# Kernel optimization log

Hardware: AMD Instinct MI355X
Metric: run time of the kernel (lower is better)

The kernel has to match this reference:

```python
import jax, jax.numpy as jnp
import numpy as np

NU, NN, NS = 50000, 20000, 2000
D_IN, D_HID, D_OUT = 128, 128, 64
LRELU_SLOPE = 0.01  # torch F.leaky_relu default


def _edges(k, n_src, n_dst, e):
    k1, k2 = jax.random.split(k)
    return (jax.random.randint(k1, (e,), 0, n_src, dtype=jnp.int32),
            jax.random.randint(k2, (e,), 0, n_dst, dtype=jnp.int32))


def setup_inputs() -> dict:
    key = jax.random.key(0)
    ks = jax.random.split(key, 32)
    fs, fd = _edges(ks[0], NU, NU, 500000)
    ps, pd = _edges(ks[1], NU, NN, 300000)
    pbs, pbd = _edges(ks[2], NN, NU, 300000)
    us, ud = _edges(ks[3], NS, NN, 150000)
    ubs, ubd = _edges(ks[4], NN, NS, 150000)
    s = 0.05
    inp = {
        "x_user": jax.random.normal(ks[5], (NU, D_IN), jnp.float32),
        "x_news": jax.random.normal(ks[6], (NN, D_IN), jnp.float32),
        "x_source": jax.random.normal(ks[7], (NS, D_IN), jnp.float32),
        # stacked per-relation GraphConv params, order:
        # [follows, posts, posted_by, publishes, published_by]
        "W1": jax.random.normal(ks[8], (5, D_IN, D_HID), jnp.float32) * s,
        "b1": jnp.zeros((5, D_HID), jnp.float32),
        "W2": jax.random.normal(ks[9], (5, D_HID, D_HID), jnp.float32) * s,
        "b2": jnp.zeros((5, D_HID), jnp.float32),
        "Wu": jax.random.normal(ks[10], (D_HID, D_OUT), jnp.float32) * s,
        "bu": jnp.zeros((D_OUT,), jnp.float32),
        "Wn": jax.random.normal(ks[11], (D_HID, D_OUT), jnp.float32) * s,
        "bn": jnp.zeros((D_OUT,), jnp.float32),
        "Ws": jax.random.normal(ks[12], (D_HID, D_OUT), jnp.float32) * s,
        "bs": jnp.zeros((D_OUT,), jnp.float32),
        "follows_src": fs, "follows_dst": fd,
        "posts_src": ps, "posts_dst": pd,
        "postedby_src": pbs, "postedby_dst": pbd,
        "publishes_src": us, "publishes_dst": ud,
        "publishedby_src": ubs, "publishedby_dst": ubd,
    }
    return inp


def _gconv(x_src, src, dst, n_dst, W, b):
    """DGL GraphConv, norm='both': D_dst^-1/2 A D_src^-1/2 X W + b."""
    n_src = x_src.shape[0]
    ones = jnp.ones(src.shape[0], x_src.dtype)
    dout = jnp.clip(jax.ops.segment_sum(ones, src, num_segments=n_src), 1.0)
    din = jnp.clip(jax.ops.segment_sum(ones, dst, num_segments=n_dst), 1.0)
    h = (x_src * jax.lax.rsqrt(dout)[:, None]) @ W  # transform before gather
    agg = jax.ops.segment_sum(h[src], dst, num_segments=n_dst)
    return agg * jax.lax.rsqrt(din)[:, None] + b


def _hetero_layer(xu, xn, xs, E, W, b):
    # mean aggregation across relations sharing a dst type
    hu = 0.5 * (_gconv(xu, E["fs"], E["fd"], NU, W[0], b[0])
                + _gconv(xn, E["pbs"], E["pbd"], NU, W[2], b[2]))
    hn = 0.5 * (_gconv(xu, E["ps"], E["pd"], NN, W[1], b[1])
                + _gconv(xs, E["us"], E["ud"], NN, W[3], b[3]))
    hs = _gconv(xn, E["ubs"], E["ubd"], NS, W[4], b[4])
    return hu, hn, hs


def reference(x_user, x_news, x_source, W1, b1, W2, b2, Wu, bu, Wn, bn, Ws, bs,
              follows_src, follows_dst, posts_src, posts_dst,
              postedby_src, postedby_dst, publishes_src, publishes_dst,
              publishedby_src, publishedby_dst):
    E = {"fs": follows_src, "fd": follows_dst, "ps": posts_src, "pd": posts_dst,
         "pbs": postedby_src, "pbd": postedby_dst, "us": publishes_src,
         "ud": publishes_dst, "ubs": publishedby_src, "ubd": publishedby_dst}
    lrelu = lambda v: jax.nn.leaky_relu(v, LRELU_SLOPE)
    hu, hn, hs = _hetero_layer(x_user, x_news, x_source, E, W1, b1)
    hu, hn, hs = lrelu(hu), lrelu(hn), lrelu(hs)
    hu, hn, hs = _hetero_layer(hu, hn, hs, E, W2, b2)
    hu, hn, hs = lrelu(hu), lrelu(hn), lrelu(hs)
    ou = hu @ Wu + bu
    on = hn @ Wn + bn
    os_ = hs @ Ws + bs
    return (ou, on, os_, hu, hn, hs)
```

## Files before the change

### kernel.cpp

```cpp
#include <hip/hip_runtime.h>

#define LRELU 0.01f

static const int kNU = 50000, kNN = 20000, kNS = 2000;
static const int DOUT_OFF[5] = {0, 100000, 170000, 240000, 262000};
static const int DIN_OFF[5]  = {50000, 150000, 190000, 242000, 282000};
static const int RP_OFF[5]   = {0, 50001, 70002, 120003, 140004};
static const int CSR_OFF[5]  = {0, 500000, 800000, 1100000, 1250000};

using bf16x8 = __attribute__((ext_vector_type(8))) short;
using u16x8  = __attribute__((ext_vector_type(8))) unsigned short;
using f32x4  = __attribute__((ext_vector_type(4))) float;

__device__ __forceinline__ float bf2f(unsigned short u) {
  return __uint_as_float(((unsigned)u) << 16);
}
__device__ __forceinline__ unsigned short f2bf(float f) {
  unsigned u = __float_as_uint(f);
  u += 0x7FFFu + ((u >> 16) & 1u);
  return (unsigned short)(u >> 16);
}


struct HArgs { const int* esrc[5]; const int* edst[5]; int* pos; int* partial; };

__global__ __launch_bounds__(512) void k_hist(HArgs a) {
  __shared__ int hbin[8192];
  int bx = blockIdx.x;
  int t = threadIdx.x;
  if (bx < 336) {
    constexpr int DSTART[6] = {0, 112, 160, 272, 320, 336};
    constexpr int NDT[5] = {50000, 20000, 50000, 20000, 2000};
    constexpr int CS[5]  = {31250, 18750, 18750, 9375, 9375};
    constexpr int EE[5]  = {500000, 300000, 300000, 150000, 150000};
    constexpr int PB[5]  = {0, 800000, 1120000, 1920000, 2240000};
    constexpr int COFF[5] = {0, 500000, 800000, 1100000, 1250000};
    int r = 0;
    while (bx >= DSTART[r + 1]) ++r;
    int local = bx - DSTART[r];
    int g = local / 16, c = local % 16;
    int nd = NDT[r];
    int gbase = g * 8192;
    int gend = gbase + 8192 < nd ? gbase + 8192 : nd;
    const int* dst = a.edst[r];
    int* pos = a.pos + COFF[r];
    int elo = c * CS[r];
    int ehi = elo + CS[r] < EE[r] ? elo + CS[r] : EE[r];
    for (int j = t; j < 8192; j += 512) hbin[j] = 0;
    __syncthreads();
    int span = ehi - elo;
    int efull = elo + (span / 4096) * 4096;
    for (int b = elo + t; b < efull; b += 4096) {
      int d[8];
#pragma unroll
      for (int k = 0; k < 8; ++k) d[k] = dst[b + k * 512];
#pragma unroll
      for (int k = 0; k < 8; ++k)
        if (d[k] >= gbase && d[k] < gend)
          pos[b + k * 512] = atomicAdd(&hbin[d[k] - gbase], 1);
    }
    for (int e = efull + t; e < ehi; e += 512) {
      int d = dst[e];
      if (d >= gbase && d < gend) pos[e] = atomicAdd(&hbin[d - gbase], 1);
    }
    __syncthreads();
    int* out = a.partial + PB[r] + (size_t)c * nd + gbase;
    int nn = gend - gbase;
    for (int j = t; j < nn; j += 512) out[j] = hbin[j];
  } else {
    constexpr int OSTART[6] = {0, 112, 224, 272, 288, 336};
    constexpr int NST[5] = {50000, 50000, 20000, 2000, 20000};
    constexpr int CS[5]  = {31250, 18750, 18750, 9375, 9375};
    constexpr int EE[5]  = {500000, 300000, 300000, 150000, 150000};
    constexpr int PB[5]  = {2272000, 3072000, 3872000, 4192000, 4224000};
    int idx = bx - 336;
    int r = 0;
    while (idx >= OSTART[r + 1]) ++r;
    int local = idx - OSTART[r];
    int g = local / 16, c = local % 16;
    int ns = NST[r];
    int gbase = g * 8192;
    int gend = gbase + 8192 < ns ? gbase + 8192 : ns;
    const int* src = a.esrc[r];
    int elo = c * CS[r];
    int ehi = elo + CS[r] < EE[r] ? elo + CS[r] : EE[r];
    for (int j = t; j < 8192; j += 512) hbin[j] = 0;
    __syncthreads();
    int span = ehi - elo;
    int efull = elo + (span / 4096) * 4096;
    for (int b = elo + t; b < efull; b += 4096) {
      int s[8];
#pragma unroll
      for (int k = 0; k < 8; ++k) s[k] = src[b + k * 512];
#pragma unroll
      for (int k = 0; k < 8; ++k)
        if (s[k] >= gbase && s[k] < gend) atomicAdd(&hbin[s[k] - gbase], 1);
    }
    for (int e = efull + t; e < ehi; e += 512) {
      int s = src[e];
      if (s >= gbase && s < gend) atomicAdd(&hbin[s - gbase], 1);
    }
    __syncthreads();
    int* out = a.partial + PB[r] + (size_t)c * ns + gbase;
    int nn = gend - gbase;
    for (int j = t; j < nn; j += 512) out[j] = hbin[j];
  }
}


struct BArgs { int* partial; int* cnt; float* rs; };

__global__ __launch_bounds__(256) void k_scanB(BArgs a) {
  int bx = blockIdx.x;
  int t = threadIdx.x;
  if (bx < 555) {
    int i = bx * 256 + t;
    if (i >= 142000) return;
    constexpr int NDT[5] = {50000, 20000, 50000, 20000, 2000};
    constexpr int PB[5]  = {0, 800000, 1120000, 1920000, 2240000};
    constexpr int DOFF[5] = {50000, 150000, 190000, 242000, 282000};
    int r, d;
    if      (i < 50000)  { r = 0; d = i; }
    else if (i < 70000)  { r = 1; d = i - 50000; }
    else if (i < 120000) { r = 2; d = i - 70000; }
    else if (i < 140000) { r = 3; d = i - 120000; }
    else                 { r = 4; d = i - 140000; }
    int nd = NDT[r];
    int* p = a.partial + PB[r] + d;
    int run = 0;
#pragma unroll
    for (int c = 0; c < 16; ++c) {
      int v = p[(size_t)c * nd];
      p[(size_t)c * nd] = run;
      run += v;
    }
    a.cnt[DOFF[r] + d] = run;
    a.rs[DOFF[r] + d] = rsqrtf((float)(run > 1 ? run : 1));
  } else {
    int i = (bx - 555) * 256 + t;
    if (i >= 142000) return;
    constexpr int NST[5] = {50000, 50000, 20000, 2000, 20000};
    constexpr int PB[5]  = {2272000, 3072000, 3872000, 4192000, 4224000};
    constexpr int OOFF[5] = {0, 100000, 170000, 240000, 262000};
    int r, s;
    if      (i < 50000)  { r = 0; s = i; }
    else if (i < 100000) { r = 1; s = i - 50000; }
    else if (i < 120000) { r = 2; s = i - 100000; }
    else if (i < 122000) { r = 3; s = i - 120000; }
    else                 { r = 4; s = i - 122000; }
    int ns = NST[r];
    const int* p = a.partial + PB[r] + s;
    int sum = 0;
#pragma unroll
    for (int c = 0; c < 16; ++c) sum += p[(size_t)c * ns];
    a.rs[OOFF[r] + s] = rsqrtf((float)(sum > 1 ? sum : 1));
  }
}


struct S3Args { const int* cnt; int* rp; };

__global__ __launch_bounds__(256) void k_scan3(S3Args a) {
  constexpr int CSTART[6] = {0, 49, 69, 118, 138, 140};
  constexpr int NDT[5] = {50000, 20000, 50000, 20000, 2000};
  constexpr int DOFF[5] = {50000, 150000, 190000, 242000, 282000};
  constexpr int RPOFF[5] = {0, 50001, 70002, 120003, 140004};
  int bx = blockIdx.x, r = 0;
  while (bx >= CSTART[r + 1]) ++r;
  int chunk = bx - CSTART[r];
  int nch = CSTART[r + 1] - CSTART[r];
  int n = NDT[r];
  const int* cnt = a.cnt + DOFF[r];
  int* rp = a.rp + RPOFF[r];
  int t = threadIdx.x;
  __shared__ int sd[256];
  __shared__ int choff_sh;
  int lim = chunk * 1024;
  int pre = 0;
  for (int j = t; j < lim; j += 256) pre += cnt[j];
  sd[t] = pre;
  __syncthreads();
  for (int off = 128; off > 0; off >>= 1) {
    if (t < off) sd[t] += sd[t + off];
    __syncthreads();
  }
  if (t == 0) choff_sh = sd[0];
  __syncthreads();
  int idx0 = lim + t * 4;
  int v[4];
#pragma unroll
  for (int j = 0; j < 4; ++j) v[j] = (idx0 + j < n) ? cnt[idx0 + j] : 0;
  int tsum = v[0] + v[1] + v[2] + v[3];
  sd[t] = tsum;
  __syncthreads();
  for (int s = 1; s < 256; s <<= 1) {
    int add = (t >= s) ? sd[t - s] : 0;
    __syncthreads();
    sd[t] += add;
    __syncthreads();
  }
  int off = choff_sh + sd[t] - tsum;
#pragma unroll
  for (int j = 0; j < 4; ++j) {
    if (idx0 + j < n) rp[idx0 + j] = off;
    off += v[j];
  }
  if (chunk == nch - 1 && t == 255) rp[n] = choff_sh + sd[255];
}


struct TJob { const float* X; const float* W; unsigned short* Y; int M; };
struct PrepJob { const float* W0; const float* W128; unsigned short* hi;
                 unsigned short* lo; int NOUT; int lgK; int bstart; };
struct CXArgs { const int* esrc[5]; const int* edst[5]; const int* pos;
                const int* rp; const int* partial; int* csr;
                TJob tj[5]; PrepJob pj[6]; };

__device__ __forceinline__ void transform_body(const TJob& p, int bxl, int t) {
  int w = t >> 6, l = t & 63;
  int lo16 = l & 15, hi4 = l >> 4;
  int m0 = bxl * 64;
  int M = p.M;
  f32x4 acc[4][2] = {};
  for (int s = 0; s < 4; ++s) {
    int kbase = s * 32 + hi4 * 8;
    bf16x8 af[4];
#pragma unroll
    for (int mf = 0; mf < 4; ++mf) {
      int row = m0 + mf * 16 + lo16;
      row = row < M ? row : M - 1;
      const float* xr = &p.X[(size_t)row * 128 + kbase];
      float4 xa = *(const float4*)xr;
      float4 xb = *(const float4*)(xr + 4);
      af[mf][0] = (short)f2bf(xa.x); af[mf][1] = (short)f2bf(xa.y);
      af[mf][2] = (short)f2bf(xa.z); af[mf][3] = (short)f2bf(xa.w);
      af[mf][4] = (short)f2bf(xb.x); af[mf][5] = (short)f2bf(xb.y);
      af[mf][6] = (short)f2bf(xb.z); af[mf][7] = (short)f2bf(xb.w);
    }
#pragma unroll
    for (int nf = 0; nf < 2; ++nf) {
      int n = (w * 2 + nf) * 16 + lo16;
      bf16x8 bh, bl;
#pragma unroll
      for (int j = 0; j < 8; ++j) {
        float wv = p.W[(size_t)(kbase + j) * 128 + n];
        unsigned short h = f2bf(wv);
        bh[j] = (short)h;
        bl[j] = (short)f2bf(wv - bf2f(h));
      }
#pragma unroll
      for (int mf = 0; mf < 4; ++mf) {
        acc[mf][nf] = __builtin_amdgcn_mfma_f32_16x16x32_bf16(af[mf], bh, acc[mf][nf], 0, 0, 0);
        acc[mf][nf] = __builtin_amdgcn_mfma_f32_16x16x32_bf16(af[mf], bl, acc[mf][nf], 0, 0, 0);
      }
    }
  }
#pragma unroll
  for (int nf = 0; nf < 2; ++nf) {
    int col = (w * 2 + nf) * 16 + lo16;
#pragma unroll
    for (int mf = 0; mf < 4; ++mf) {
#pragma unroll
      for (int rr = 0; rr < 4; ++rr) {
        int row = m0 + mf * 16 + hi4 * 4 + rr;
        if (row < M) p.Y[(size_t)row * 128 + col] = f2bf(acc[mf][nf][rr]);
      }
    }
  }
}

__global__ __launch_bounds__(256) void k_buildCx(CXArgs a) {
  int bx = blockIdx.x;
  int t = threadIdx.x;
  int g = bx / 3, m = bx % 3;
  if (m == 0) {
    constexpr int ESTART[6] = {0, 489, 782, 1075, 1222, 1369};
    constexpr int NDT[5] = {50000, 20000, 50000, 20000, 2000};
    constexpr int CS[5]  = {31250, 18750, 18750, 9375, 9375};
    constexpr int EE[5]  = {500000, 300000, 300000, 150000, 150000};
    constexpr int PB[5]  = {0, 800000, 1120000, 1920000, 2240000};
    constexpr int RPOFF[5] = {0, 50001, 70002, 120003, 140004};
    constexpr int COFF[5] = {0, 500000, 800000, 1100000, 1250000};
    int idx = g;
    if (idx >= 1369) return;
    int r = 0;
    while (idx >= ESTART[r + 1]) ++r;
    int i0 = (idx - ESTART[r]) * 1024 + t;
    const int* edst = a.edst[r];
    const int* esrc = a.esrc[r];
    const int* pos = a.pos + COFF[r];
    const int* rp = a.rp + RPOFF[r];
    const int* pb = a.partial + PB[r];
    int* csr = a.csr + COFF[r];
    int E = EE[r], cs = CS[r], nd = NDT[r];
    int i[4], d[4];
    bool v[4];
#pragma unroll
    for (int k = 0; k < 4; ++k) {
      i[k] = i0 + k * 256;
      v[k] = i[k] < E;
      d[k] = v[k] ? edst[i[k]] : 0;
    }
    int slot[4];
#pragma unroll
    for (int k = 0; k < 4; ++k) {
      if (v[k]) {
        int c = i[k] / cs;
        slot[k] = rp[d[k]] + pb[(size_t)c * nd + d[k]] + pos[i[k]];
      }
    }
#pragma unroll
    for (int k = 0; k < 4; ++k)
      if (v[k]) csr[slot[k]] = esrc[i[k]];
  } else {
    int idx = g * 2 + (m - 1);
    if (idx < 2222) {
      constexpr int TSTART[6] = {0, 782, 1564, 1877, 1909, 2222};
      int r = 0;
      while (idx >= TSTART[r + 1]) ++r;
      transform_body(a.tj[r], idx - TSTART[r], t);
    } else if (idx < 2638) {
      int b = idx - 2222, ji = 0;
      while (ji < 5 && b >= a.pj[ji + 1].bstart) ++ji;
      PrepJob p = a.pj[ji];
      int eidx = (b - p.bstart) * 256 + t;
      int K = 1 << p.lgK;
      int n = eidx >> p.lgK, k = eidx & (K - 1);
      if (n >= p.NOUT) return;
      float w = (k < 128) ? p.W0[k * p.NOUT + n] : p.W128[(k - 128) * p.NOUT + n];
      unsigned short h = f2bf(w);
      float res = w - bf2f(h);
      p.hi[n * K + k] = h;
      p.lo[n * K + k] = f2bf(res);
    }
  }
}


#define GROW(vv, cc)                                                              \
  _Pragma("unroll") for (int q = 0; q < 8; ++q)                                   \
      acc[q] = fmaf(__uint_as_float(((unsigned)(unsigned short)vv[q]) << 16), cc, acc[q]);

__device__ __forceinline__ void gat_accum(const int* __restrict__ rp,
    const int* __restrict__ csr, const unsigned short* __restrict__ Y,
    const float* __restrict__ rso, int wid, int sub, float* acc) {
  int e0 = rp[wid], e1 = rp[wid + 1];
  for (int base = e0; base < e1; base += 16) {
    int m = e1 - base;
    if (m > 16) m = 16;
    int ei = base + (sub < m ? sub : 0);
    int se = csr[ei];
    float sc = (sub < m) ? rso[se] : 0.f;
    bf16x8 v[16];
#pragma unroll
    for (int j = 0; j < 16; ++j) {
      int sj = __shfl(se, j, 16);
      v[j] = *(const bf16x8*)&Y[(size_t)sj * 128 + sub * 8];
    }
#pragma unroll
    for (int j = 0; j < 16; ++j) {
      float cj = __shfl(sc, j, 16);
      GROW(v[j], cj)
    }
  }
}


struct G1Rel { const int* rp; const int* csr; const unsigned short* Y;
               const float* rso; const float* rsi; };
struct G1Args { G1Rel rel[5]; const float* b;
                unsigned short* hU; unsigned short* hN; unsigned short* hS; };

__global__ __launch_bounds__(256) void k_gather1(G1Args a) {
  int bx = blockIdx.x;
  int t = threadIdx.x;
  int sub = t & 15;
  float acc[8], tot[8];
#pragma unroll
  for (int q = 0; q < 8; ++q) acc[q] = 0.f;
  if (bx < 3125) {
    int wid = bx * 16 + (t >> 4);
    gat_accum(a.rel[0].rp, a.rel[0].csr, a.rel[0].Y, a.rel[0].rso, wid, sub, acc);
    float s0 = a.rel[0].rsi[wid];
#pragma unroll
    for (int q = 0; q < 8; ++q) { tot[q] = s0 * acc[q]; acc[q] = 0.f; }
    gat_accum(a.rel[2].rp, a.rel[2].csr, a.rel[2].Y, a.rel[2].rso, wid, sub, acc);
    float s2 = a.rel[2].rsi[wid];
    const float* b0 = a.b;
    const float* b2 = a.b + 2 * 128;
    u16x8 o;
#pragma unroll
    for (int q = 0; q < 8; ++q) {
      float v = 0.5f * (tot[q] + s2 * acc[q] + b0[sub * 8 + q] + b2[sub * 8 + q]);
      v = v >= 0.f ? v : LRELU * v;
      o[q] = f2bf(v);
    }
    *(u16x8*)&a.hU[(size_t)wid * 128 + sub * 8] = o;
  } else if (bx < 4375) {
    int wid = (bx - 3125) * 16 + (t >> 4);
    gat_accum(a.rel[1].rp, a.rel[1].csr, a.rel[1].Y, a.rel[1].rso, wid, sub, acc);
    float s1 = a.rel[1].rsi[wid];
#pragma unroll
    for (int q = 0; q < 8; ++q) { tot[q] = s1 * acc[q]; acc[q] = 0.f; }
    gat_accum(a.rel[3].rp, a.rel[3].csr, a.rel[3].Y, a.rel[3].rso, wid, sub, acc);
    float s3 = a.rel[3].rsi[wid];
    const float* b1v = a.b + 128;
    const float* b3 = a.b + 3 * 128;
    u16x8 o;
#pragma unroll
    for (int q = 0; q < 8; ++q) {
      float v = 0.5f * (tot[q] + s3 * acc[q] + b1v[sub * 8 + q] + b3[sub * 8 + q]);
      v = v >= 0.f ? v : LRELU * v;
      o[q] = f2bf(v);
    }
    *(u16x8*)&a.hN[(size_t)wid * 128 + sub * 8] = o;
  } else {
    int wid = (bx - 4375) * 16 + (t >> 4);
    gat_accum(a.rel[4].rp, a.rel[4].csr, a.rel[4].Y, a.rel[4].rso, wid, sub, acc);
    float s4 = a.rel[4].rsi[wid];
    const float* b4 = a.b + 4 * 128;
    u16x8 o;
#pragma unroll
    for (int q = 0; q < 8; ++q) {
      float v = s4 * acc[q] + b4[sub * 8 + q];
      v = v >= 0.f ? v : LRELU * v;
      o[q] = f2bf(v);
    }
    *(u16x8*)&a.hS[(size_t)wid * 128 + sub * 8] = o;
  }
}


struct GMJob {
  const int* rpA; const int* csrA; const unsigned short* YA;
  const float* rsoA; const float* rsiA;
  const int* rpB; const int* csrB; const unsigned short* YB;
  const float* rsoB; const float* rsiB;
  const unsigned short* Wh; const unsigned short* Wl;
  const float* b0; const float* b1; float scale;
  float* H; unsigned short* Hb; int M; int KP;
};
struct GMArgs { GMJob j[3]; };

__global__ __launch_bounds__(512) void k_gmm(GMArgs a) {
  __shared__ unsigned short As[64 * 256];
  int bx = blockIdx.x;
  int ji, bxl;
  if (bx < 782)       { ji = 0; bxl = bx; }
  else if (bx < 1095) { ji = 1; bxl = bx - 782; }
  else                { ji = 2; bxl = bx - 1095; }
  const GMJob& p = a.j[ji];
  int t = threadIdx.x;
  int m0 = bxl * 64;
  char* asb = (char*)As;
  int sub = t & 15;
  int rowloc = t >> 4;
  for (int half = 0; half < 2; ++half) {
    int rl = rowloc + half * 32;
    int wid = m0 + rl;
    bool ok = wid < p.M;
    {
      float acc[8];
#pragma unroll
      for (int q = 0; q < 8; ++q) acc[q] = 0.f;
      float si = 0.f;
      if (ok) { gat_accum(p.rpA, p.csrA, p.YA, p.rsoA, wid, sub, acc); si = p.rsiA[wid]; }
      u16x8 o;
#pragma unroll
      for (int q = 0; q < 8; ++q) o[q] = f2bf(acc[q] * si);
      int cb = sub * 16;
      *(u16x8*)(asb + rl * 512 + (cb ^ ((rl & 7) << 4))) = o;
    }
    if (p.rpB) {
      float acc[8];
#pragma unroll
      for (int q = 0; q < 8; ++q) acc[q] = 0.f;
      float si = 0.f;
      if (ok) { gat_accum(p.rpB, p.csrB, p.YB, p.rsoB, wid, sub, acc); si = p.rsiB[wid]; }
      u16x8 o;
#pragma unroll
      for (int q = 0; q < 8; ++q) o[q] = f2bf(acc[q] * si);
      int cb = 256 + sub * 16;
      *(u16x8*)(asb + rl * 512 + (cb ^ ((rl & 7) << 4))) = o;
    }
  }
  __syncthreads();
  int w = t >> 6, l = t & 63;
  int lo16 = l & 15, hi4 = l >> 4;
  int KP = p.KP;
  f32x4 acc[4] = {};
  for (int s = 0; s < KP / 32; ++s) {
    int kbase = s * 32 + hi4 * 8;
    int cb = kbase * 2;
    bf16x8 af[4];
#pragma unroll
    for (int mf = 0; mf < 4; ++mf) {
      int row = mf * 16 + lo16;
      af[mf] = *(const bf16x8*)(asb + row * 512 + (cb ^ ((row & 7) << 4)));
    }
    int n = w * 16 + lo16;
    bf16x8 bh = *(const bf16x8*)&p.Wh[(size_t)n * KP + kbase];
    bf16x8 bl = *(const bf16x8*)&p.Wl[(size_t)n * KP + kbase];
#pragma unroll
    for (int mf = 0; mf < 4; ++mf) {
      acc[mf] = __builtin_amdgcn_mfma_f32_16x16x32_bf16(af[mf], bh, acc[mf], 0, 0, 0);
      acc[mf] = __builtin_amdgcn_mfma_f32_16x16x32_bf16(af[mf], bl, acc[mf], 0, 0, 0);
    }
  }
  int col = w * 16 + lo16;
  float bs = p.b0[col];
  if (p.b1) bs += p.b1[col];
#pragma unroll
  for (int mf = 0; mf < 4; ++mf) {
#pragma unroll
    for (int rr = 0; rr < 4; ++rr) {
      int row = m0 + mf * 16 + hi4 * 4 + rr;
      if (row < p.M) {
        float o = p.scale * (acc[mf][rr] + bs);
        o = o >= 0.f ? o : LRELU * o;
        p.H[(size_t)row * 128 + col] = o;
        p.Hb[(size_t)row * 128 + col] = f2bf(o);
      }
    }
  }
}


struct MJob { const unsigned short* A; const unsigned short* Wh; const unsigned short* Wl;
              const float* b0; const float* b1; float scale; int lrelu;
              float* H; int ldh; unsigned short* Hb; int M; int bstart; };
struct MArgs { MJob j[3]; };

template <int KCH, int NW>
__device__ __forceinline__ void mgemm_body(const MJob& p, int bxl) {
  constexpr int KP = KCH * 128;
  int t = threadIdx.x;
  int w = t >> 6, l = t & 63;
  int lo16 = l & 15, hi4 = l >> 4;
  int m0 = bxl * 64;
  int M = p.M;
  const unsigned short* A = p.A;
  f32x4 acc[4][NW] = {};
  for (int s = 0; s < KP / 32; ++s) {
    int kbase = s * 32 + hi4 * 8;
    bf16x8 af[4];
#pragma unroll
    for (int mf = 0; mf < 4; ++mf) {
      int row = m0 + mf * 16 + lo16;
      row = row < M ? row : M - 1;
      af[mf] = *(const bf16x8*)&A[(size_t)row * KP + kbase];
    }
#pragma unroll
    for (int nf = 0; nf < NW; ++nf) {
      int n = (w * NW + nf) * 16 + lo16;
      bf16x8 bh = *(const bf16x8*)&p.Wh[(size_t)n * KP + kbase];
      bf16x8 bl = *(const bf16x8*)&p.Wl[(size_t)n * KP + kbase];
#pragma unroll
      for (int mf = 0; mf < 4; ++mf) {
        acc[mf][nf] = __builtin_amdgcn_mfma_f32_16x16x32_bf16(af[mf], bh, acc[mf][nf], 0, 0, 0);
        acc[mf][nf] = __builtin_amdgcn_mfma_f32_16x16x32_bf16(af[mf], bl, acc[mf][nf], 0, 0, 0);
      }
    }
  }
#pragma unroll
  for (int nf = 0; nf < NW; ++nf) {
    int col = (w * NW + nf) * 16 + lo16;
    float bs = p.b0 ? p.b0[col] : 0.f;
    if (p.b1) bs += p.b1[col];
#pragma unroll
    for (int mf = 0; mf < 4; ++mf) {
#pragma unroll
      for (int rr = 0; rr < 4; ++rr) {
        int row = m0 + mf * 16 + hi4 * 4 + rr;
        if (row < M) {
          float o = p.scale * (acc[mf][nf][rr] + bs);
          if (p.lrelu) o = o >= 0.f ? o : LRELU * o;
          if (p.H) p.H[(size_t)row * p.ldh + col] = o;
          if (p.Hb) p.Hb[(size_t)row * p.ldh + col] = f2bf(o);
        }
      }
    }
  }
}

__global__ __launch_bounds__(256) void k_proj3(MArgs a) {
  int bx = blockIdx.x;
  if (bx < a.j[1].bstart)      mgemm_body<1, 1>(a.j[0], bx);
  else if (bx < a.j[2].bstart) mgemm_body<1, 1>(a.j[1], bx - a.j[1].bstart);
  else                         mgemm_body<1, 1>(a.j[2], bx - a.j[2].bstart);
}


extern "C" void kernel_launch(void* const* d_in, const int* in_sizes, int n_in,
                              void* d_out, int out_size, void* d_ws, size_t ws_size,
                              hipStream_t stream) {
  const float* xu = (const float*)d_in[0];
  const float* xn = (const float*)d_in[1];
  const float* xs = (const float*)d_in[2];
  const float* W1 = (const float*)d_in[3];
  const float* b1 = (const float*)d_in[4];
  const float* W2 = (const float*)d_in[5];
  const float* b2 = (const float*)d_in[6];
  const float* Wu = (const float*)d_in[7];
  const float* bu = (const float*)d_in[8];
  const float* Wn = (const float*)d_in[9];
  const float* bn = (const float*)d_in[10];
  const float* Wsrc = (const float*)d_in[11];
  const float* bsrc = (const float*)d_in[12];
  const int* SRC[5] = {(const int*)d_in[13], (const int*)d_in[15], (const int*)d_in[17],
                       (const int*)d_in[19], (const int*)d_in[21]};
  const int* DST[5] = {(const int*)d_in[14], (const int*)d_in[16], (const int*)d_in[18],
                       (const int*)d_in[20], (const int*)d_in[22]};

  int* ws_i = (int*)d_ws;
  int* rp = ws_i;
  int* csr = ws_i + 142008;
  int* pos = ws_i + 1542008;
  int* cnt = ws_i + 2942328;
  float* rs = (float*)(ws_i + 3226328);
  unsigned short* wt = (unsigned short*)(rs + 284000);
  unsigned short* h2bU = wt + 376832;
  unsigned short* h2bN = h2bU + 6400000;
  unsigned short* h2bS = h2bN + 2560000;
  unsigned short* xbU = wt + 376832 + 18176000;
  unsigned short* xbN = xbU + 6400000;
  unsigned short* xbS = xbN + 2560000;

  unsigned short* L2U_h = wt + 163840, * L2U_l = wt + 196608;
  unsigned short* L2N_h = wt + 229376, * L2N_l = wt + 262144;
  unsigned short* L2S_h = wt + 294912, * L2S_l = wt + 311296;
  unsigned short* PU_h = wt + 327680, * PU_l = wt + 335872;
  unsigned short* PN_h = wt + 344064, * PN_l = wt + 352256;
  unsigned short* PS_h = wt + 360448, * PS_l = wt + 368640;

  float* outf = (float*)d_out;
  float* ou = outf;
  float* on = outf + 3200000;
  float* osrc = outf + 4480000;
  float* hu = outf + 4608000;
  float* hn = outf + 11008000;
  float* hs = outf + 13568000;

  int* partial = (int*)outf;

  unsigned short* Yb = (unsigned short*)(outf + 4608000);
  unsigned short* Y0 = Yb;
  unsigned short* Y1 = Y0 + 6400000;
  unsigned short* Y2a = Y1 + 6400000;
  unsigned short* Y3 = Y2a + 2560000;
  unsigned short* Y4 = Y3 + 256000;

  HArgs ha;
  for (int r = 0; r < 5; ++r) { ha.esrc[r] = SRC[r]; ha.edst[r] = DST[r]; }
  ha.pos = pos;
  ha.partial = partial;
  k_hist<<<672, 512, 0, stream>>>(ha);

  BArgs ba = {partial, cnt, rs};
  k_scanB<<<1110, 256, 0, stream>>>(ba);

  S3Args s3 = {cnt, rp};
  k_scan3<<<140, 256, 0, stream>>>(s3);

  CXArgs ca;
  for (int r = 0; r < 5; ++r) { ca.esrc[r] = SRC[r]; ca.edst[r] = DST[r]; }
  ca.pos = pos;
  ca.rp = rp;
  ca.partial = partial;
  ca.csr = csr;
  ca.tj[0] = {xu, W1 + 0 * 16384, Y0, kNU};
  ca.tj[1] = {xu, W1 + 1 * 16384, Y1, kNU};
  ca.tj[2] = {xn, W1 + 2 * 16384, Y2a, kNN};
  ca.tj[3] = {xs, W1 + 3 * 16384, Y3, kNS};
  ca.tj[4] = {xn, W1 + 4 * 16384, Y4, kNN};
  ca.pj[0] = {W2, W2 + 2 * 16384, L2U_h, L2U_l, 128, 8, 0};
  ca.pj[1] = {W2 + 16384, W2 + 3 * 16384, L2N_h, L2N_l, 128, 8, 128};
  ca.pj[2] = {W2 + 4 * 16384, nullptr, L2S_h, L2S_l, 128, 7, 256};
  ca.pj[3] = {Wu, nullptr, PU_h, PU_l, 64, 7, 320};
  ca.pj[4] = {Wn, nullptr, PN_h, PN_l, 64, 7, 352};
  ca.pj[5] = {Wsrc, nullptr, PS_h, PS_l, 64, 7, 384};
  k_buildCx<<<4107, 256, 0, stream>>>(ca);

  G1Args g1;
  const unsigned short* YT[5] = {Y0, Y1, Y2a, Y3, Y4};
  for (int r = 0; r < 5; ++r)
    g1.rel[r] = {rp + RP_OFF[r], csr + CSR_OFF[r], YT[r],
                 rs + DOUT_OFF[r], rs + DIN_OFF[r]};
  g1.b = b1;
  g1.hU = xbU; g1.hN = xbN; g1.hS = xbS;
  k_gather1<<<4500, 256, 0, stream>>>(g1);

  GMArgs gm;
  gm.j[0] = {rp + RP_OFF[0], csr + CSR_OFF[0], xbU, rs + DOUT_OFF[0], rs + DIN_OFF[0],
             rp + RP_OFF[2], csr + CSR_OFF[2], xbN, rs + DOUT_OFF[2], rs + DIN_OFF[2],
             L2U_h, L2U_l, b2, b2 + 2 * 128, 0.5f, hu, h2bU, kNU, 256};
  gm.j[1] = {rp + RP_OFF[1], csr + CSR_OFF[1], xbU, rs + DOUT_OFF[1], rs + DIN_OFF[1],
             rp + RP_OFF[3], csr + CSR_OFF[3], xbS, rs + DOUT_OFF[3], rs + DIN_OFF[3],
             L2N_h, L2N_l, b2 + 128, b2 + 3 * 128, 0.5f, hn, h2bN, kNN, 256};
  gm.j[2] = {rp + RP_OFF[4], csr + CSR_OFF[4], xbN, rs + DOUT_OFF[4], rs + DIN_OFF[4],
             nullptr, nullptr, nullptr, nullptr, nullptr,
             L2S_h, L2S_l, b2 + 4 * 128, nullptr, 1.0f, hs, h2bS, kNS, 128};
  k_gmm<<<1127, 512, 0, stream>>>(gm);

  MArgs pm;
  pm.j[0] = {h2bU, PU_h, PU_l, bu, nullptr, 1.0f, 0, ou, 64, nullptr, kNU, 0};
  pm.j[1] = {h2bN, PN_h, PN_l, bn, nullptr, 1.0f, 0, on, 64, nullptr, kNN, 782};
  pm.j[2] = {h2bS, PS_h, PS_l, bsrc, nullptr, 1.0f, 0, osrc, 64, nullptr, kNS, 1095};
  k_proj3<<<1127, 256, 0, stream>>>(pm);
}
```

Measured before the change: 307.0 us.

## Interleave paired-relation gathers and fold row offsets into partial counts

Adds gat_pair, which issues the first 16-edge gather loads for two relations together before accumulating either, so more independent memory loads are in flight per thread in both the layer-1 aggregation and the fused gather-GEMM. It also makes k_scan3 add each destination's row-pointer offset into the per-chunk partial counts, so CSR construction reads one array per edge instead of two. The cost is higher register pressure from holding 32 bf16x8 vectors, which may lower occupancy, plus extra read-modify-write traffic over the partial array in the scan kernel.

After: 330.8 us. 1.08x slower.

```diff
diff --git a/kernel.cpp b/kernel.cpp
--- a/kernel.cpp
+++ b/kernel.cpp
@@ -158,13 +158,14 @@
 }
 
 
-struct S3Args { const int* cnt; int* rp; };
+struct S3Args { const int* cnt; int* rp; int* partial; };
 
 __global__ __launch_bounds__(256) void k_scan3(S3Args a) {
   constexpr int CSTART[6] = {0, 49, 69, 118, 138, 140};
   constexpr int NDT[5] = {50000, 20000, 50000, 20000, 2000};
   constexpr int DOFF[5] = {50000, 150000, 190000, 242000, 282000};
   constexpr int RPOFF[5] = {0, 50001, 70002, 120003, 140004};
+  constexpr int PB[5]  = {0, 800000, 1120000, 1920000, 2240000};
   int bx = blockIdx.x, r = 0;
   while (bx >= CSTART[r + 1]) ++r;
   int chunk = bx - CSTART[r];
@@ -200,12 +201,21 @@
     __syncthreads();
   }
   int off = choff_sh + sd[t] - tsum;
+  int st[4];
 #pragma unroll
   for (int j = 0; j < 4; ++j) {
+    st[j] = off;
     if (idx0 + j < n) rp[idx0 + j] = off;
     off += v[j];
   }
   if (chunk == nch - 1 && t == 255) rp[n] = choff_sh + sd[255];
+  int* pb = a.partial + PB[r];
+  for (int c = 0; c < 16; ++c) {
+    size_t base = (size_t)c * n;
+#pragma unroll
+    for (int j = 0; j < 4; ++j)
+      if (idx0 + j < n) pb[base + idx0 + j] += st[j];
+  }
 }
 
 
@@ -213,7 +223,7 @@
 struct PrepJob { const float* W0; const float* W128; unsigned short* hi;
                  unsigned short* lo; int NOUT; int lgK; int bstart; };
 struct CXArgs { const int* esrc[5]; const int* edst[5]; const int* pos;
-                const int* rp; const int* partial; int* csr;
+                const int* partial; int* csr;
                 TJob tj[5]; PrepJob pj[6]; };
 
 __device__ __forceinline__ void transform_body(const TJob& p, int bxl, int t) {
@@ -279,7 +289,6 @@
     constexpr int CS[5]  = {31250, 18750, 18750, 9375, 9375};
     constexpr int EE[5]  = {500000, 300000, 300000, 150000, 150000};
     constexpr int PB[5]  = {0, 800000, 1120000, 1920000, 2240000};
-    constexpr int RPOFF[5] = {0, 50001, 70002, 120003, 140004};
     constexpr int COFF[5] = {0, 500000, 800000, 1100000, 1250000};
     int idx = g;
     if (idx >= 1369) return;
@@ -289,7 +298,6 @@
     const int* edst = a.edst[r];
     const int* esrc = a.esrc[r];
     const int* pos = a.pos + COFF[r];
-    const int* rp = a.rp + RPOFF[r];
     const int* pb = a.partial + PB[r];
     int* csr = a.csr + COFF[r];
     int E = EE[r], cs = CS[r], nd = NDT[r];
@@ -306,7 +314,7 @@
     for (int k = 0; k < 4; ++k) {
       if (v[k]) {
         int c = i[k] / cs;
-        slot[k] = rp[d[k]] + pb[(size_t)c * nd + d[k]] + pos[i[k]];
+        slot[k] = pb[(size_t)c * nd + d[k]] + pos[i[k]];
       }
     }
 #pragma unroll
@@ -341,10 +349,9 @@
   _Pragma("unroll") for (int q = 0; q < 8; ++q)                                   \
       acc[q] = fmaf(__uint_as_float(((unsigned)(unsigned short)vv[q]) << 16), cc, acc[q]);
 
-__device__ __forceinline__ void gat_accum(const int* __restrict__ rp,
+__device__ __forceinline__ void gat_range(int e0, int e1,
     const int* __restrict__ csr, const unsigned short* __restrict__ Y,
-    const float* __restrict__ rso, int wid, int sub, float* acc) {
-  int e0 = rp[wid], e1 = rp[wid + 1];
+    const float* __restrict__ rso, int sub, float* acc) {
   for (int base = e0; base < e1; base += 16) {
     int m = e1 - base;
     if (m > 16) m = 16;
@@ -365,6 +372,53 @@
   }
 }
 
+__device__ __forceinline__ void gat_accum(const int* __restrict__ rp,
+    const int* __restrict__ csr, const unsigned short* __restrict__ Y,
+    const float* __restrict__ rso, int wid, int sub, float* acc) {
+  gat_range(rp[wid], rp[wid + 1], csr, Y, rso, sub, acc);
+}
+
+__device__ __forceinline__ void gat_pair(
+    const int* __restrict__ rpA, const int* __restrict__ csrA,
+    const unsigned short* __restrict__ YA, const float* __restrict__ rsoA,
+    const int* __restrict__ rpB, const int* __restrict__ csrB,
+    const unsigned short* __restrict__ YB, const float* __restrict__ rsoB,
+    int wid, int sub, float* accA, float* accB) {
+  int a0 = rpA[wid], a1 = rpA[wid + 1];
+  int b0 = rpB[wid], b1 = rpB[wid + 1];
+  int ma = a1 - a0; ma = ma > 16 ? 16 : ma;
+  int mb = b1 - b0; mb = mb > 16 ? 16 : mb;
+  int seA = 0, seB = 0;
+  float scA = 0.f, scB = 0.f;
+  if (sub < ma) { seA = csrA[a0 + sub]; scA = rsoA[seA]; }
+  if (sub < mb) { seB = csrB[b0 + sub]; scB = rsoB[seB]; }
+  bf16x8 vA[16], vB[16];
+#pragma unroll
+  for (int j = 0; j < 16; ++j) {
+    int sj = __shfl(seA, j, 16);
+    vA[j] = *(const bf16x8*)&YA[(size_t)sj * 128 + sub * 8];
+  }
+#pragma unroll
+  for (int j = 0; j < 16; ++j) {
+    int sj = __shfl(seB, j, 16);
+    vB[j] = *(const bf16x8*)&YB[(size_t)sj * 128 + sub * 8];
+  }
+#pragma unroll
+  for (int j = 0; j < 16; ++j) {
+    float cj = __shfl(scA, j, 16);
+    float* acc = accA;
+    GROW(vA[j], cj)
+  }
+#pragma unroll
+  for (int j = 0; j < 16; ++j) {
+    float cj = __shfl(scB, j, 16);
+    float* acc = accB;
+    GROW(vB[j], cj)
+  }
+  if (a0 + 16 < a1) gat_range(a0 + 16, a1, csrA, YA, rsoA, sub, accA);
+  if (b0 + 16 < b1) gat_range(b0 + 16, b1, csrB, YB, rsoB, sub, accB);
+}
+
 
 struct G1Rel { const int* rp; const int* csr; const unsigned short* Y;
                const float* rso; const float* rsi; };
@@ -375,54 +429,52 @@
   int bx = blockIdx.x;
   int t = threadIdx.x;
   int sub = t & 15;
-  float acc[8], tot[8];
-#pragma unroll
-  for (int q = 0; q < 8; ++q) acc[q] = 0.f;
+  float accA[8], accB[8];
+#pragma unroll
+  for (int q = 0; q < 8; ++q) { accA[q] = 0.f; accB[q] = 0.f; }
   if (bx < 3125) {
     int wid = bx * 16 + (t >> 4);
-    gat_accum(a.rel[0].rp, a.rel[0].csr, a.rel[0].Y, a.rel[0].rso, wid, sub, acc);
+    gat_pair(a.rel[0].rp, a.rel[0].csr, a.rel[0].Y, a.rel[0].rso,
+             a.rel[2].rp, a.rel[2].csr, a.rel[2].Y, a.rel[2].rso,
+             wid, sub, accA, accB);
     float s0 = a.rel[0].rsi[wid];
-#pragma unroll
-    for (int q = 0; q < 8; ++q) { tot[q] = s0 * acc[q]; acc[q] = 0.f; }
-    gat_accum(a.rel[2].rp, a.rel[2].csr, a.rel[2].Y, a.rel[2].rso, wid, sub, acc);
     float s2 = a.rel[2].rsi[wid];
     const float* b0 = a.b;
     const float* b2 = a.b + 2 * 128;
     u16x8 o;
 #pragma unroll
     for (int q = 0; q < 8; ++q) {
-      float v = 0.5f * (tot[q] + s2 * acc[q] + b0[sub * 8 + q] + b2[sub * 8 + q]);
+      float v = 0.5f * (s0 * accA[q] + s2 * accB[q] + b0[sub * 8 + q] + b2[sub * 8 + q]);
       v = v >= 0.f ? v : LRELU * v;
       o[q] = f2bf(v);
     }
     *(u16x8*)&a.hU[(size_t)wid * 128 + sub * 8] = o;
   } else if (bx < 4375) {
     int wid = (bx - 3125) * 16 + (t >> 4);
-    gat_accum(a.rel[1].rp, a.rel[1].csr, a.rel[1].Y, a.rel[1].rso, wid, sub, acc);
+    gat_pair(a.rel[1].rp, a.rel[1].csr, a.rel[1].Y, a.rel[1].rso,
+             a.rel[3].rp, a.rel[3].csr, a.rel[3].Y, a.rel[3].rso,
+             wid, sub, accA, accB);
     float s1 = a.rel[1].rsi[wid];
-#pragma unroll
-    for (int q = 0; q < 8; ++q) { tot[q] = s1 * acc[q]; acc[q] = 0.f; }
-    gat_accum(a.rel[3].rp, a.rel[3].csr, a.rel[3].Y, a.rel[3].rso, wid, sub, acc);
     float s3 = a.rel[3].rsi[wid];
     const float* b1v = a.b + 128;
     const float* b3 = a.b + 3 * 128;
     u16x8 o;
 #pragma unroll
     for (int q = 0; q < 8; ++q) {
-      float v = 0.5f * (tot[q] + s3 * acc[q] + b1v[sub * 8 + q] + b3[sub * 8 + q]);
+      float v = 0.5f * (s1 * accA[q] + s3 * accB[q] + b1v[sub * 8 + q] + b3[sub * 8 + q]);
       v = v >= 0.f ? v : LRELU * v;
       o[q] = f2bf(v);
     }
     *(u16x8*)&a.hN[(size_t)wid * 128 + sub * 8] = o;
   } else {
     int wid = (bx - 4375) * 16 + (t >> 4);
-    gat_accum(a.rel[4].rp, a.rel[4].csr, a.rel[4].Y, a.rel[4].rso, wid, sub, acc);
+    gat_accum(a.rel[4].rp, a.rel[4].csr, a.rel[4].Y, a.rel[4].rso, wid, sub, accA);
     float s4 = a.rel[4].rsi[wid];
     const float* b4 = a.b + 4 * 128;
     u16x8 o;
 #pragma unroll
     for (int q = 0; q < 8; ++q) {
-      float v = s4 * acc[q] + b4[sub * 8 + q];
+      float v = s4 * accA[q] + b4[sub * 8 + q];
       v = v >= 0.f ? v : LRELU * v;
       o[q] = f2bf(v);
     }
@@ -459,29 +511,31 @@
     int rl = rowloc + half * 32;
     int wid = m0 + rl;
     bool ok = wid < p.M;
-    {
-      float acc[8];
-#pragma unroll
-      for (int q = 0; q < 8; ++q) acc[q] = 0.f;
-      float si = 0.f;
-      if (ok) { gat_accum(p.rpA, p.csrA, p.YA, p.rsoA, wid, sub, acc); si = p.rsiA[wid]; }
-      u16x8 o;
-#pragma unroll
-      for (int q = 0; q < 8; ++q) o[q] = f2bf(acc[q] * si);
-      int cb = sub * 16;
-      *(u16x8*)(asb + rl * 512 + (cb ^ ((rl & 7) << 4))) = o;
-    }
+    float accA[8], accB[8];
+#pragma unroll
+    for (int q = 0; q < 8; ++q) { accA[q] = 0.f; accB[q] = 0.f; }
+    float siA = 0.f, siB = 0.f;
     if (p.rpB) {
-      float acc[8];
-#pragma unroll
-      for (int q = 0; q < 8; ++q) acc[q] = 0.f;
-      float si = 0.f;
-      if (ok) { gat_accum(p.rpB, p.csrB, p.YB, p.rsoB, wid, sub, acc); si = p.rsiB[wid]; }
-      u16x8 o;
-#pragma unroll
-      for (int q = 0; q < 8; ++q) o[q] = f2bf(acc[q] * si);
-      int cb = 256 + sub * 16;
-      *(u16x8*)(asb + rl * 512 + (cb ^ ((rl & 7) << 4))) = o;
+      if (ok) {
+        gat_pair(p.rpA, p.csrA, p.YA, p.rsoA, p.rpB, p.csrB, p.YB, p.rsoB,
+                 wid, sub, accA, accB);
+        siA = p.rsiA[wid];
+        siB = p.rsiB[wid];
+      }
+      u16x8 oA, oB;
+#pragma unroll
+      for (int q = 0; q < 8; ++q) { oA[q] = f2bf(accA[q] * siA); oB[q] = f2bf(accB[q] * siB); }
+      int cbA = sub * 16;
+      int cbB = 256 + sub * 16;
+      *(u16x8*)(asb + rl * 512 + (cbA ^ ((rl & 7) << 4))) = oA;
+      *(u16x8*)(asb + rl * 512 + (cbB ^ ((rl & 7) << 4))) = oB;
+    } else {
+      if (ok) { gat_accum(p.rpA, p.csrA, p.YA, p.rsoA, wid, sub, accA); siA = p.rsiA[wid]; }
+      u16x8 oA;
+#pragma unroll
+      for (int q = 0; q < 8; ++q) oA[q] = f2bf(accA[q] * siA);
+      int cbA = sub * 16;
+      *(u16x8*)(asb + rl * 512 + (cbA ^ ((rl & 7) << 4))) = oA;
     }
   }
   __syncthreads();
@@ -659,13 +713,12 @@
   BArgs ba = {partial, cnt, rs};
   k_scanB<<<1110, 256, 0, stream>>>(ba);
 
-  S3Args s3 = {cnt, rp};
+  S3Args s3 = {cnt, rp, partial};
   k_scan3<<<140, 256, 0, stream>>>(s3);
 
   CXArgs ca;
   for (int r = 0; r < 5; ++r) { ca.esrc[r] = SRC[r]; ca.edst[r] = DST[r]; }
   ca.pos = pos;
-  ca.rp = rp;
   ca.partial = partial;
   ca.csr = csr;
   ca.tj[0] = {xu, W1 + 0 * 16384, Y0, kNU};
```
